# Optimization experiments

Measured on AMD Instinct MI355X. Metric: run time of the kernel, lower is better.

## Reference

```python
import jax, jax.numpy as jnp
import numpy as np

STRIDES = (8, 16, 32)
BINS = 16
NC = 80
ALPHA, GAMMA = 0.25, 2.0
W_CLS, W_IOU, W_DFL = 1.0, 7.5, 1.5
B, MAX_GT = 32, 32
EPS = 1e-7


def setup_inputs() -> dict:
    key = jax.random.key(0)
    k0, k1, k2, k3, k4, k5, k6 = jax.random.split(key, 7)
    p0 = jax.random.normal(k0, (B, 4 * BINS + NC, 80, 80), dtype=jnp.float32)
    p1 = jax.random.normal(k1, (B, 4 * BINS + NC, 40, 40), dtype=jnp.float32)
    p2 = jax.random.normal(k2, (B, 4 * BINS + NC, 20, 20), dtype=jnp.float32)
    # realistic xyxy boxes inside a 640x640 image
    c = jax.random.uniform(k3, (B, MAX_GT, 2), minval=60.0, maxval=580.0)
    wh = jax.random.uniform(k4, (B, MAX_GT, 2), minval=16.0, maxval=120.0)
    gt_bboxes = jnp.concatenate([c - wh / 2, c + wh / 2], axis=-1).astype(jnp.float32)
    gt_labels = jax.random.randint(k5, (B, MAX_GT), 0, NC, dtype=jnp.int32)
    raw = jax.random.randint(k6, (B, 8400), 0, 20 * MAX_GT, dtype=jnp.int32)
    matched_gt_inds = jnp.where(raw < MAX_GT, raw, -1)
    return {"p0": p0, "p1": p1, "p2": p2, "gt_bboxes": gt_bboxes,
            "gt_labels": gt_labels, "matched_gt_inds": matched_gt_inds}


def _decode_scale(p, stride):
    # p: [B, 4*BINS + NC, H, W]
    Bp, C, H, W = p.shape
    dfl = p[:, :4 * BINS].reshape(Bp, 4, BINS, H, W)
    cls = p[:, 4 * BINS:]
    # DFL decode: expectation of softmax over bins, scaled by stride
    prob = jax.nn.softmax(dfl, axis=2)
    proj = jnp.arange(BINS, dtype=p.dtype)
    dist = jnp.einsum('bkchw,c->bkhw', prob, proj) * stride  # [B,4,H,W] in pixels
    ys, xs = jnp.meshgrid(jnp.arange(H), jnp.arange(W), indexing='ij')
    cx = ((xs.astype(p.dtype)) + 0.5) * stride
    cy = ((ys.astype(p.dtype)) + 0.5) * stride
    boxes = jnp.stack([cx - dist[:, 0], cy - dist[:, 1],
                       cx + dist[:, 2], cy + dist[:, 3]], axis=-1).reshape(Bp, H * W, 4)
    cls_logits = cls.transpose(0, 2, 3, 1).reshape(Bp, H * W, NC)
    dfl_flat = dfl.transpose(0, 3, 4, 1, 2).reshape(Bp, H * W, 4, BINS)
    grid = jnp.stack([cx, cy], axis=-1).reshape(H * W, 2)
    smap = jnp.full((H * W,), stride, dtype=p.dtype)
    return cls_logits, dfl_flat, boxes, grid, smap


def reference(p0, p1, p2, gt_bboxes, gt_labels, matched_gt_inds):
    outs = [_decode_scale(p, s) for p, s in zip((p0, p1, p2), STRIDES)]
    scores = jnp.concatenate([o[0] for o in outs], axis=1)   # [B,N,NC]
    dfl = jnp.concatenate([o[1] for o in outs], axis=1)      # [B,N,4,BINS]
    pboxes = jnp.concatenate([o[2] for o in outs], axis=1)   # [B,N,4]
    grid = jnp.concatenate([o[3] for o in outs], axis=0)     # [N,2]
    smap = jnp.concatenate([o[4] for o in outs], axis=0)     # [N]

    pos = matched_gt_inds >= 0                               # [B,N]
    idx = jnp.where(pos, matched_gt_inds, 0)
    lbl = jnp.take_along_axis(gt_labels, idx, axis=1)        # [B,N]
    posf = pos.astype(scores.dtype)
    tgt_scores = jax.nn.one_hot(lbl, NC, dtype=scores.dtype) * posf[..., None]

    # sigmoid focal loss (stable BCE-with-logits)
    prob = jax.nn.sigmoid(scores)
    ce = jnp.maximum(scores, 0) - scores * tgt_scores + jnp.log1p(jnp.exp(-jnp.abs(scores)))
    p_t = prob * tgt_scores + (1 - prob) * (1 - tgt_scores)
    alpha_t = tgt_scores * ALPHA + (1 - tgt_scores) * (1 - ALPHA)
    cls_elem = alpha_t * (1.0 - p_t) ** GAMMA * ce
    num_pos = jnp.maximum(posf.sum(), 1.0)
    loss_cls = cls_elem.sum() / num_pos

    # gather matched GT boxes per anchor
    tboxes = jnp.take_along_axis(gt_bboxes, idx[..., None], axis=1)  # [B,N,4]
    gx, gy = grid[None, :, 0], grid[None, :, 1]
    l = jnp.clip(gx - tboxes[..., 0], 0.0)
    t = jnp.clip(gy - tboxes[..., 1], 0.0)
    r = jnp.clip(tboxes[..., 2] - gx, 0.0)
    b_ = jnp.clip(tboxes[..., 3] - gy, 0.0)
    dists = jnp.stack([l, t, r, b_], axis=-1) / smap[None, :, None]   # [B,N,4]
    tb = jnp.clip(dists, 0.0, BINS - 1 - 1e-6)
    lo = jnp.floor(tb).astype(jnp.int32)
    hi = jnp.minimum(lo + 1, BINS - 1)
    a = tb - lo.astype(tb.dtype)
    # soft two-bin DFL target (vectorized form of the scatter_add loop)
    tdist = (jax.nn.one_hot(lo, BINS, dtype=dfl.dtype) * (1.0 - a)[..., None]
             + jax.nn.one_hot(hi, BINS, dtype=dfl.dtype) * a[..., None])   # [B,N,4,BINS]
    logp = jax.nn.log_softmax(dfl, axis=-1)
    dfl_elem = -(tdist * logp).sum(-1)                                # [B,N,4]
    loss_dfl = (dfl_elem * posf[..., None]).sum() / (num_pos * 4.0)

    # IoU loss on positives
    ix1 = jnp.maximum(pboxes[..., 0], tboxes[..., 0])
    iy1 = jnp.maximum(pboxes[..., 1], tboxes[..., 1])
    ix2 = jnp.minimum(pboxes[..., 2], tboxes[..., 2])
    iy2 = jnp.minimum(pboxes[..., 3], tboxes[..., 3])
    inter = jnp.clip(ix2 - ix1, 0.0) * jnp.clip(iy2 - iy1, 0.0)
    area_p = jnp.clip(pboxes[..., 2] - pboxes[..., 0], 0.0) * jnp.clip(pboxes[..., 3] - pboxes[..., 1], 0.0)
    area_t = jnp.clip(tboxes[..., 2] - tboxes[..., 0], 0.0) * jnp.clip(tboxes[..., 3] - tboxes[..., 1], 0.0)
    iou = inter / (area_p + area_t - inter + EPS)
    loss_iou = ((1.0 - iou) * posf).sum() / num_pos

    total = W_CLS * loss_cls + W_IOU * loss_iou + W_DFL * loss_dfl
    return total
```

## Files before the change

kernel.cpp:

```cpp
#include <hip/hip_runtime.h>
#include <math.h>

#define NCLS 80
#define BINS 16
#define BATCH 32
#define MAX_GT 32
#define NA 8400
#define AN (BATCH * NA)
#define NT 2100
#define NB_CLS 5120
#define NB_DFL 525
#define DFL_THREADS (NB_DFL * 256)
#define NSLOT 64
#define ALPHA_C 0.25f
#define W_CLS 1.0
#define W_IOU 7.5
#define W_DFL 1.5
#define EPS_F 1e-7f


__device__ __forceinline__ void block_reduce_atomic(float val, double* __restrict__ target)
{
    __shared__ float s[4];
    __syncthreads();
    #pragma unroll
    for (int o = 32; o > 0; o >>= 1) val += __shfl_down(val, o);
    const int wave = threadIdx.x >> 6, lane = threadIdx.x & 63;
    if (lane == 0) s[wave] = val;
    __syncthreads();
    if (threadIdx.x == 0) atomicAdd(target, (double)(s[0] + s[1] + s[2] + s[3]));
}

__global__ __launch_bounds__(256) void yolo_prep(
    const int* __restrict__ matched, const int* __restrict__ gt_labels,
    signed char* __restrict__ lblmap)
{
    const int qid = blockIdx.x * 256 + threadIdx.x;
    if (qid >= AN / 4) return;
    const int a0 = qid * 4;
    const int b  = a0 / NA;
    const int4 m4 = *(const int4*)(matched + a0);
    const int mm[4] = {m4.x, m4.y, m4.z, m4.w};
    char4 o;
    o.x = (mm[0] >= 0) ? (signed char)gt_labels[b * MAX_GT + mm[0]] : (signed char)-1;
    o.y = (mm[1] >= 0) ? (signed char)gt_labels[b * MAX_GT + mm[1]] : (signed char)-1;
    o.z = (mm[2] >= 0) ? (signed char)gt_labels[b * MAX_GT + mm[2]] : (signed char)-1;
    o.w = (mm[3] >= 0) ? (signed char)gt_labels[b * MAX_GT + mm[3]] : (signed char)-1;
    *(char4*)(lblmap + a0) = o;
}

__global__ __launch_bounds__(256) void yolo_mega(
    const float* __restrict__ p0, const float* __restrict__ p1, const float* __restrict__ p2,
    const float* __restrict__ gt_bboxes, const int* __restrict__ matched,
    const signed char* __restrict__ lblmap,
    float* __restrict__ pdist, double* __restrict__ acc)
{
    const int bid  = blockIdx.x;
    const int slot = bid & (NSLOT - 1);
    float part = 0.f;

    if (bid < NB_CLS) {
        const int plane = bid >> 1;
        const int b = plane / NCLS;
        const int c = plane - b * NCLS;

        for (int t = (bid & 1) * 256 + (int)threadIdx.x; t < NT; t += 512) {
            const float* p; int HW, off, gbase;
            if (t < 1600)      { p = p0; HW = 6400; off = t * 4;          gbase = 0;    }
            else if (t < 2000) { p = p1; HW = 1600; off = (t - 1600) * 4; gbase = 6400; }
            else               { p = p2; HW = 400;  off = (t - 2000) * 4; gbase = 8000; }

            float4 q = *(const float4*)(p + (size_t)(b * 144 + 4 * BINS + c) * HW + off);
            char4 l4 = *(const char4*)(lblmap + b * NA + gbase + off);
            const int   lbl[4] = {l4.x, l4.y, l4.z, l4.w};
            const float s4[4]  = {q.x, q.y, q.z, q.w};
            #pragma unroll
            for (int j = 0; j < 4; ++j) {
                float s  = s4[j];
                float tt = (c == lbl[j]) ? 1.f : 0.f;
                float e   = __expf(-fabsf(s));
                float inv = 1.f / (1.f + e);
                float prob = (s >= 0.f) ? inv : e * inv;
                float ce  = fmaxf(s, 0.f) - s * tt + __logf(1.f + e);
                float p_t = prob * tt + (1.f - prob) * (1.f - tt);
                float alpha_t = tt * ALPHA_C + (1.f - tt) * (1.f - ALPHA_C);
                float om = 1.f - p_t;
                part += alpha_t * om * om * ce;
            }
        }
        block_reduce_atomic(part, &acc[0 * NSLOT + slot]);
    } else {
        const int dt0 = (bid - NB_CLS) * 256 + (int)threadIdx.x;
        #pragma unroll
        for (int rep = 0; rep < 2; ++rep) {
            const int it = dt0 + rep * DFL_THREADS;
            const int t  = it % NT;
            const int r  = it / NT;
            const int b  = r & 31;
            const int k  = r >> 5;

            const float* p; int HW, off, gbase, h, w0; float stride;
            if (t < 1600)      { p = p0; HW = 6400; off = t * 4;          gbase = 0;    stride = 8.f;
                                 h = t / 20;  w0 = (t - h * 20) * 4; }
            else if (t < 2000) { p = p1; HW = 1600; off = (t - 1600) * 4; gbase = 6400; stride = 16.f;
                                 int u = t - 1600; h = u / 10; w0 = (u - h * 10) * 4; }
            else               { p = p2; HW = 400;  off = (t - 2000) * 4; gbase = 8000; stride = 32.f;
                                 int u = t - 2000; h = u / 5;  w0 = (u - h * 5) * 4; }
            const float inv_s = 1.f / stride;
            const float cy = ((float)h + 0.5f) * stride;

            const int4 m4 = *(const int4*)(matched + (size_t)b * NA + gbase + off);
            const int mm[4] = {m4.x, m4.y, m4.z, m4.w};

            float tdv[4]; bool pos[4];
            #pragma unroll
            for (int j = 0; j < 4; ++j) {
                pos[j] = (mm[j] >= 0);
                int idx = pos[j] ? mm[j] : 0;
                float4 tb = *(const float4*)(gt_bboxes + ((size_t)b * MAX_GT + idx) * 4);
                float cx = ((float)(w0 + j) + 0.5f) * stride;
                float d = (k == 0) ? (cx - tb.x) : (k == 1) ? (cy - tb.y)
                        : (k == 2) ? (tb.z - cx) : (tb.w - cy);
                tdv[j] = fmaxf(d, 0.f) * inv_s;
            }

            const float* pc = p + (size_t)(b * 144 + k * BINS) * HW + off;
            float v[BINS][4];
            #pragma unroll
            for (int i = 0; i < BINS; ++i) {
                float4 q = *(const float4*)(pc + (size_t)i * HW);
                v[i][0] = q.x; v[i][1] = q.y; v[i][2] = q.z; v[i][3] = q.w;
            }

            float pd[4];
            #pragma unroll
            for (int j = 0; j < 4; ++j) {
                float tval = fminf(tdv[j], (float)(BINS - 1) - 1e-6f);
                int   lo = (int)floorf(tval);
                float fr = tval - (float)lo;

                float mx = v[0][j];
                #pragma unroll
                for (int i = 1; i < BINS; ++i) mx = fmaxf(mx, v[i][j]);

                float se = 0.f, we = 0.f, vlo = 0.f, vhi = 0.f;
                #pragma unroll
                for (int i = 0; i < BINS; ++i) {
                    float e = __expf(v[i][j] - mx);
                    se += e;
                    we += (float)i * e;
                    vlo = (i == lo)     ? v[i][j] : vlo;
                    vhi = (i == lo + 1) ? v[i][j] : vhi;
                }
                pd[j] = (we / se) * stride;
                if (pos[j]) {
                    float lse = mx + __logf(se);
                    part += -((1.f - fr) * (vlo - lse) + fr * (vhi - lse));
                }
            }
            float4 st = {pd[0], pd[1], pd[2], pd[3]};
            *(float4*)(pdist + (size_t)k * AN + (size_t)b * NA + gbase + off) = st;
        }
        block_reduce_atomic(part, &acc[2 * NSLOT + slot]);
    }
}

__global__ __launch_bounds__(256) void yolo_iou(
    const float* __restrict__ gt_bboxes, const int* __restrict__ matched,
    const float* __restrict__ pdist, double* __restrict__ acc)
{
    const int t = blockIdx.x * 256 + threadIdx.x;
    const int b = blockIdx.y;
    const int slot = (blockIdx.x + blockIdx.y * 9) & (NSLOT - 1);

    float iou_acc = 0.f, cnt = 0.f;

    if (t < NT) {
        int HW, W, off, gbase; float stride;
        if (t < 1600)      { HW = 6400; W = 80; stride = 8.f;  off = t * 4;          gbase = 0;    }
        else if (t < 2000) { HW = 1600; W = 40; stride = 16.f; off = (t - 1600) * 4; gbase = 6400; }
        else               { HW = 400;  W = 20; stride = 32.f; off = (t - 2000) * 4; gbase = 8000; }

        const int h  = off / W;
        const int w0 = off - h * W;
        const float cy = ((float)h + 0.5f) * stride;

        const int4 m4 = *(const int4*)(matched + (size_t)b * NA + gbase + off);
        const int mm[4] = {m4.x, m4.y, m4.z, m4.w};

        float pdj[4][4];
        #pragma unroll
        for (int k = 0; k < 4; ++k) {
            float4 q = *(const float4*)(pdist + (size_t)k * AN + (size_t)b * NA + gbase + off);
            pdj[k][0] = q.x; pdj[k][1] = q.y; pdj[k][2] = q.z; pdj[k][3] = q.w;
        }

        #pragma unroll
        for (int j = 0; j < 4; ++j) {
            if (mm[j] >= 0) {
                float4 tb = *(const float4*)(gt_bboxes + ((size_t)b * MAX_GT + mm[j]) * 4);
                float cx = ((float)(w0 + j) + 0.5f) * stride;
                float px1 = cx - pdj[0][j], py1 = cy - pdj[1][j];
                float px2 = cx + pdj[2][j], py2 = cy + pdj[3][j];
                float ix1 = fmaxf(px1, tb.x), iy1 = fmaxf(py1, tb.y);
                float ix2 = fminf(px2, tb.z), iy2 = fminf(py2, tb.w);
                float inter  = fmaxf(ix2 - ix1, 0.f) * fmaxf(iy2 - iy1, 0.f);
                float area_p = fmaxf(px2 - px1, 0.f) * fmaxf(py2 - py1, 0.f);
                float area_t = fmaxf(tb.z - tb.x, 0.f) * fmaxf(tb.w - tb.y, 0.f);
                float iou = inter / (area_p + area_t - inter + EPS_F);
                iou_acc += 1.f - iou;
                cnt += 1.f;
            }
        }
    }
    block_reduce_atomic(iou_acc, &acc[1 * NSLOT + slot]);
    block_reduce_atomic(cnt,     &acc[3 * NSLOT + slot]);
}

__global__ __launch_bounds__(256) void yolo_loss_fused(
    const float* __restrict__ p0, const float* __restrict__ p1, const float* __restrict__ p2,
    const float* __restrict__ gt_bboxes, const int* __restrict__ gt_labels,
    const int* __restrict__ matched, double* __restrict__ acc)
{
    const int a = blockIdx.x * blockDim.x + threadIdx.x;
    const int b = blockIdx.y;
    const int slot = blockIdx.x & (NSLOT - 1);
    float cls_acc = 0.f, iou_acc = 0.f, dfl_acc = 0.f, pos_cnt = 0.f;
    if (a < NA) {
        const float* p; int HW, W; float stride; int off;
        if (a < 6400)      { p = p0; HW = 6400; W = 80; stride = 8.f;  off = a; }
        else if (a < 8000) { p = p1; HW = 1600; W = 40; stride = 16.f; off = a - 6400; }
        else               { p = p2; HW = 400;  W = 20; stride = 32.f; off = a - 8000; }
        const int h = off / W, w = off - h * W;
        const float cx = ((float)w + 0.5f) * stride, cy = ((float)h + 0.5f) * stride;
        const float* pb = p + ((size_t)b * 144) * (size_t)HW + (size_t)off;
        const int m = matched[(size_t)b * NA + a];
        const bool pos = (m >= 0);
        const int idx = pos ? m : 0;
        const int lbl = gt_labels[b * MAX_GT + idx];
        const float* tbp = gt_bboxes + ((size_t)b * MAX_GT + idx) * 4;
        const float tx1 = tbp[0], ty1 = tbp[1], tx2 = tbp[2], ty2 = tbp[3];
        float tdist[4] = {fmaxf(cx - tx1, 0.f) / stride, fmaxf(cy - ty1, 0.f) / stride,
                          fmaxf(tx2 - cx, 0.f) / stride, fmaxf(ty2 - cy, 0.f) / stride};
        float pdv[4]; float dfl_sum = 0.f;
        #pragma unroll
        for (int k = 0; k < 4; ++k) {
            float tv = fminf(tdist[k], (float)(BINS - 1) - 1e-6f);
            int lo = (int)floorf(tv);
            float fr = tv - (float)lo;
            const float* pc = pb + (size_t)(k * BINS) * HW;
            float v[BINS];
            #pragma unroll
            for (int i = 0; i < BINS; ++i) v[i] = pc[(size_t)i * HW];
            float mx = v[0];
            #pragma unroll
            for (int i = 1; i < BINS; ++i) mx = fmaxf(mx, v[i]);
            float se = 0.f, we = 0.f, vlo = 0.f, vhi = 0.f;
            #pragma unroll
            for (int i = 0; i < BINS; ++i) {
                float e = __expf(v[i] - mx);
                se += e; we += (float)i * e;
                vlo = (i == lo) ? v[i] : vlo;
                vhi = (i == lo + 1) ? v[i] : vhi;
            }
            pdv[k] = (we / se) * stride;
            if (pos) { float lse = mx + __logf(se); dfl_sum += -((1.f - fr) * (vlo - lse) + fr * (vhi - lse)); }
        }
        const float* pcls = pb + (size_t)(4 * BINS) * HW;
        #pragma unroll 4
        for (int c = 0; c < NCLS; ++c) {
            float s = pcls[(size_t)c * HW];
            float tt = (pos && c == lbl) ? 1.f : 0.f;
            float e = __expf(-fabsf(s));
            float inv = 1.f / (1.f + e);
            float prob = (s >= 0.f) ? inv : e * inv;
            float ce = fmaxf(s, 0.f) - s * tt + __logf(1.f + e);
            float p_t = prob * tt + (1.f - prob) * (1.f - tt);
            float alpha_t = tt * ALPHA_C + (1.f - tt) * (1.f - ALPHA_C);
            float om = 1.f - p_t;
            cls_acc += alpha_t * om * om * ce;
        }
        if (pos) {
            float px1 = cx - pdv[0], py1 = cy - pdv[1], px2 = cx + pdv[2], py2 = cy + pdv[3];
            float ix1 = fmaxf(px1, tx1), iy1 = fmaxf(py1, ty1);
            float ix2 = fminf(px2, tx2), iy2 = fminf(py2, ty2);
            float inter  = fmaxf(ix2 - ix1, 0.f) * fmaxf(iy2 - iy1, 0.f);
            float area_p = fmaxf(px2 - px1, 0.f) * fmaxf(py2 - py1, 0.f);
            float area_t = fmaxf(tx2 - tx1, 0.f) * fmaxf(ty2 - ty1, 0.f);
            float iou = inter / (area_p + area_t - inter + EPS_F);
            iou_acc = 1.f - iou; dfl_acc = dfl_sum; pos_cnt = 1.f;
        }
    }
    block_reduce_atomic(cls_acc, &acc[0 * NSLOT + slot]);
    block_reduce_atomic(iou_acc, &acc[1 * NSLOT + slot]);
    block_reduce_atomic(dfl_acc, &acc[2 * NSLOT + slot]);
    block_reduce_atomic(pos_cnt, &acc[3 * NSLOT + slot]);
}

__global__ void yolo_loss_finalize(const double* __restrict__ acc, float* __restrict__ out)
{
    double s[4] = {0.0, 0.0, 0.0, 0.0};
    for (int q = 0; q < 4; ++q)
        for (int i = 0; i < NSLOT; ++i) s[q] += acc[q * NSLOT + i];
    double np = s[3] < 1.0 ? 1.0 : s[3];
    double total = W_CLS * s[0] / np + W_IOU * s[1] / np + W_DFL * s[2] / (np * 4.0);
    out[0] = (float)total;
}

extern "C" void kernel_launch(void* const* d_in, const int* in_sizes, int n_in,
                              void* d_out, int out_size, void* d_ws, size_t ws_size,
                              hipStream_t stream)
{
    const float* p0        = (const float*)d_in[0];
    const float* p1        = (const float*)d_in[1];
    const float* p2        = (const float*)d_in[2];
    const float* gt_bboxes = (const float*)d_in[3];
    const int*   gt_labels = (const int*)d_in[4];
    const int*   matched   = (const int*)d_in[5];
    float*  out = (float*)d_out;

    const size_t accBytes   = 4 * NSLOT * sizeof(double);
    const size_t pdistBytes = (size_t)4 * AN * sizeof(float);
    double*      acc    = (double*)d_ws;
    float*       pdist  = (float*)((char*)d_ws + accBytes);
    signed char* lblmap = (signed char*)((char*)d_ws + accBytes + pdistBytes);
    const size_t need = accBytes + pdistBytes + (size_t)AN;

    (void)hipMemsetAsync(acc, 0, accBytes, stream);

    if (ws_size >= need) {
        yolo_prep<<<(AN / 4 + 255) / 256, 256, 0, stream>>>(matched, gt_labels, lblmap);
        yolo_mega<<<NB_CLS + NB_DFL, 256, 0, stream>>>(p0, p1, p2, gt_bboxes, matched,
                                                       lblmap, pdist, acc);
        dim3 g2((NT + 255) / 256, BATCH);
        yolo_iou<<<g2, 256, 0, stream>>>(gt_bboxes, matched, pdist, acc);
    } else {
        dim3 g((NA + 255) / 256, BATCH);
        yolo_loss_fused<<<g, 256, 0, stream>>>(p0, p1, p2, gt_bboxes, gt_labels, matched, acc);
    }
    yolo_loss_finalize<<<1, 1, 0, stream>>>(acc, out);
}
```

Before: 229.4 us.

## Fuse IoU into DFL blocks via shared memory, drop pdist buffer and memset

```diff
diff --git a/kernel.cpp b/kernel.cpp
--- a/kernel.cpp
+++ b/kernel.cpp
@@ -8,9 +8,8 @@
 #define NA 8400
 #define AN (BATCH * NA)
 #define NT 2100
-#define NB_CLS 5120
-#define NB_DFL 525
-#define DFL_THREADS (NB_DFL * 256)
+#define NB_DFL 1050
+#define NB_CLS 2560
 #define NSLOT 64
 #define ALPHA_C 0.25f
 #define W_CLS 1.0
@@ -31,10 +30,23 @@
     if (threadIdx.x == 0) atomicAdd(target, (double)(s[0] + s[1] + s[2] + s[3]));
 }
 
+__device__ __forceinline__ float focal_elem(float s, float tt)
+{
+    float e   = __expf(-fabsf(s));
+    float inv = 1.f / (1.f + e);
+    float prob = (s >= 0.f) ? inv : e * inv;
+    float ce  = fmaxf(s, 0.f) - s * tt + __logf(1.f + e);
+    float p_t = prob * tt + (1.f - prob) * (1.f - tt);
+    float alpha_t = tt * ALPHA_C + (1.f - tt) * (1.f - ALPHA_C);
+    float om = 1.f - p_t;
+    return alpha_t * om * om * ce;
+}
+
 __global__ __launch_bounds__(256) void yolo_prep(
     const int* __restrict__ matched, const int* __restrict__ gt_labels,
-    signed char* __restrict__ lblmap)
-{
+    signed char* __restrict__ lblmap, double* __restrict__ acc)
+{
+    if (blockIdx.x == 0) acc[threadIdx.x] = 0.0;
     const int qid = blockIdx.x * 256 + threadIdx.x;
     if (qid >= AN / 4) return;
     const int a0 = qid * 4;
@@ -52,169 +64,144 @@
 __global__ __launch_bounds__(256) void yolo_mega(
     const float* __restrict__ p0, const float* __restrict__ p1, const float* __restrict__ p2,
     const float* __restrict__ gt_bboxes, const int* __restrict__ matched,
-    const signed char* __restrict__ lblmap,
-    float* __restrict__ pdist, double* __restrict__ acc)
+    const signed char* __restrict__ lblmap, double* __restrict__ acc)
 {
     const int bid  = blockIdx.x;
     const int slot = bid & (NSLOT - 1);
-    float part = 0.f;
-
-    if (bid < NB_CLS) {
-        const int plane = bid >> 1;
-        const int b = plane / NCLS;
-        const int c = plane - b * NCLS;
-
-        for (int t = (bid & 1) * 256 + (int)threadIdx.x; t < NT; t += 512) {
-            const float* p; int HW, off, gbase;
-            if (t < 1600)      { p = p0; HW = 6400; off = t * 4;          gbase = 0;    }
-            else if (t < 2000) { p = p1; HW = 1600; off = (t - 1600) * 4; gbase = 6400; }
-            else               { p = p2; HW = 400;  off = (t - 2000) * 4; gbase = 8000; }
-
-            float4 q = *(const float4*)(p + (size_t)(b * 144 + 4 * BINS + c) * HW + off);
-            char4 l4 = *(const char4*)(lblmap + b * NA + gbase + off);
-            const int   lbl[4] = {l4.x, l4.y, l4.z, l4.w};
-            const float s4[4]  = {q.x, q.y, q.z, q.w};
+
+    if (bid < NB_DFL) {
+        __shared__ float spd[64][4][4];
+        const int gdt = bid * 256 + (int)threadIdx.x;
+        const int k   = gdt & 3;
+        const int qg  = gdt >> 2;
+        const int b   = qg / NT;
+        const int t   = qg - b * NT;
+
+        const float* p; int HW, off, gbase, h, w0; float stride;
+        if (t < 1600)      { p = p0; HW = 6400; off = t * 4;          gbase = 0;    stride = 8.f;
+                             h = t / 20;  w0 = (t - h * 20) * 4; }
+        else if (t < 2000) { p = p1; HW = 1600; off = (t - 1600) * 4; gbase = 6400; stride = 16.f;
+                             int u = t - 1600; h = u / 10; w0 = (u - h * 10) * 4; }
+        else               { p = p2; HW = 400;  off = (t - 2000) * 4; gbase = 8000; stride = 32.f;
+                             int u = t - 2000; h = u / 5;  w0 = (u - h * 5) * 4; }
+        const float inv_s = 1.f / stride;
+        const float cy = ((float)h + 0.5f) * stride;
+
+        const float* pc = p + (size_t)(b * 144 + k * BINS) * HW + off;
+        float v[BINS][4];
+        #pragma unroll
+        for (int i = 0; i < BINS; ++i) {
+            float4 q = *(const float4*)(pc + (size_t)i * HW);
+            v[i][0] = q.x; v[i][1] = q.y; v[i][2] = q.z; v[i][3] = q.w;
+        }
+        const int4 m4 = *(const int4*)(matched + (size_t)b * NA + gbase + off);
+        const int mm[4] = {m4.x, m4.y, m4.z, m4.w};
+        bool pos[4]; float4 tbv[4]; float tdv[4];
+        #pragma unroll
+        for (int j = 0; j < 4; ++j) {
+            pos[j] = (mm[j] >= 0);
+            int idx = pos[j] ? mm[j] : 0;
+            tbv[j] = *(const float4*)(gt_bboxes + ((size_t)b * MAX_GT + idx) * 4);
+            float cx = ((float)(w0 + j) + 0.5f) * stride;
+            float d = (k == 0) ? (cx - tbv[j].x) : (k == 1) ? (cy - tbv[j].y)
+                    : (k == 2) ? (tbv[j].z - cx) : (tbv[j].w - cy);
+            tdv[j] = fmaxf(d, 0.f) * inv_s;
+        }
+
+        float part = 0.f;
+        float pd[4];
+        #pragma unroll
+        for (int j = 0; j < 4; ++j) {
+            float tval = fminf(tdv[j], (float)(BINS - 1) - 1e-6f);
+            int   lo = (int)floorf(tval);
+            float fr = tval - (float)lo;
+            float mx = v[0][j];
+            #pragma unroll
+            for (int i = 1; i < BINS; ++i) mx = fmaxf(mx, v[i][j]);
+            float se = 0.f, we = 0.f, vlo = 0.f, vhi = 0.f;
+            #pragma unroll
+            for (int i = 0; i < BINS; ++i) {
+                float e = __expf(v[i][j] - mx);
+                se += e;
+                we += (float)i * e;
+                vlo = (i == lo)     ? v[i][j] : vlo;
+                vhi = (i == lo + 1) ? v[i][j] : vhi;
+            }
+            pd[j] = (we / se) * stride;
+            if (pos[j]) {
+                float lse = mx + __logf(se);
+                part += -((1.f - fr) * (vlo - lse) + fr * (vhi - lse));
+            }
+        }
+        *(float4*)&spd[threadIdx.x >> 2][k][0] = make_float4(pd[0], pd[1], pd[2], pd[3]);
+        __syncthreads();
+
+        float iou_part = 0.f, cnt = 0.f;
+        if (k == 0) {
+            const int g = threadIdx.x >> 2;
             #pragma unroll
             for (int j = 0; j < 4; ++j) {
-                float s  = s4[j];
-                float tt = (c == lbl[j]) ? 1.f : 0.f;
-                float e   = __expf(-fabsf(s));
-                float inv = 1.f / (1.f + e);
-                float prob = (s >= 0.f) ? inv : e * inv;
-                float ce  = fmaxf(s, 0.f) - s * tt + __logf(1.f + e);
-                float p_t = prob * tt + (1.f - prob) * (1.f - tt);
-                float alpha_t = tt * ALPHA_C + (1.f - tt) * (1.f - ALPHA_C);
-                float om = 1.f - p_t;
-                part += alpha_t * om * om * ce;
-            }
-        }
-        block_reduce_atomic(part, &acc[0 * NSLOT + slot]);
-    } else {
-        const int dt0 = (bid - NB_CLS) * 256 + (int)threadIdx.x;
-        #pragma unroll
-        for (int rep = 0; rep < 2; ++rep) {
-            const int it = dt0 + rep * DFL_THREADS;
-            const int t  = it % NT;
-            const int r  = it / NT;
-            const int b  = r & 31;
-            const int k  = r >> 5;
-
-            const float* p; int HW, off, gbase, h, w0; float stride;
-            if (t < 1600)      { p = p0; HW = 6400; off = t * 4;          gbase = 0;    stride = 8.f;
-                                 h = t / 20;  w0 = (t - h * 20) * 4; }
-            else if (t < 2000) { p = p1; HW = 1600; off = (t - 1600) * 4; gbase = 6400; stride = 16.f;
-                                 int u = t - 1600; h = u / 10; w0 = (u - h * 10) * 4; }
-            else               { p = p2; HW = 400;  off = (t - 2000) * 4; gbase = 8000; stride = 32.f;
-                                 int u = t - 2000; h = u / 5;  w0 = (u - h * 5) * 4; }
-            const float inv_s = 1.f / stride;
-            const float cy = ((float)h + 0.5f) * stride;
-
-            const int4 m4 = *(const int4*)(matched + (size_t)b * NA + gbase + off);
-            const int mm[4] = {m4.x, m4.y, m4.z, m4.w};
-
-            float tdv[4]; bool pos[4];
-            #pragma unroll
-            for (int j = 0; j < 4; ++j) {
-                pos[j] = (mm[j] >= 0);
-                int idx = pos[j] ? mm[j] : 0;
-                float4 tb = *(const float4*)(gt_bboxes + ((size_t)b * MAX_GT + idx) * 4);
-                float cx = ((float)(w0 + j) + 0.5f) * stride;
-                float d = (k == 0) ? (cx - tb.x) : (k == 1) ? (cy - tb.y)
-                        : (k == 2) ? (tb.z - cx) : (tb.w - cy);
-                tdv[j] = fmaxf(d, 0.f) * inv_s;
-            }
-
-            const float* pc = p + (size_t)(b * 144 + k * BINS) * HW + off;
-            float v[BINS][4];
-            #pragma unroll
-            for (int i = 0; i < BINS; ++i) {
-                float4 q = *(const float4*)(pc + (size_t)i * HW);
-                v[i][0] = q.x; v[i][1] = q.y; v[i][2] = q.z; v[i][3] = q.w;
-            }
-
-            float pd[4];
-            #pragma unroll
-            for (int j = 0; j < 4; ++j) {
-                float tval = fminf(tdv[j], (float)(BINS - 1) - 1e-6f);
-                int   lo = (int)floorf(tval);
-                float fr = tval - (float)lo;
-
-                float mx = v[0][j];
-                #pragma unroll
-                for (int i = 1; i < BINS; ++i) mx = fmaxf(mx, v[i][j]);
-
-                float se = 0.f, we = 0.f, vlo = 0.f, vhi = 0.f;
-                #pragma unroll
-                for (int i = 0; i < BINS; ++i) {
-                    float e = __expf(v[i][j] - mx);
-                    se += e;
-                    we += (float)i * e;
-                    vlo = (i == lo)     ? v[i][j] : vlo;
-                    vhi = (i == lo + 1) ? v[i][j] : vhi;
-                }
-                pd[j] = (we / se) * stride;
                 if (pos[j]) {
-                    float lse = mx + __logf(se);
-                    part += -((1.f - fr) * (vlo - lse) + fr * (vhi - lse));
+                    float cx = ((float)(w0 + j) + 0.5f) * stride;
+                    float px1 = cx - spd[g][0][j], py1 = cy - spd[g][1][j];
+                    float px2 = cx + spd[g][2][j], py2 = cy + spd[g][3][j];
+                    float4 tb = tbv[j];
+                    float ix1 = fmaxf(px1, tb.x), iy1 = fmaxf(py1, tb.y);
+                    float ix2 = fminf(px2, tb.z), iy2 = fminf(py2, tb.w);
+                    float inter  = fmaxf(ix2 - ix1, 0.f) * fmaxf(iy2 - iy1, 0.f);
+                    float area_p = fmaxf(px2 - px1, 0.f) * fmaxf(py2 - py1, 0.f);
+                    float area_t = fmaxf(tb.z - tb.x, 0.f) * fmaxf(tb.w - tb.y, 0.f);
+                    float iou = inter / (area_p + area_t - inter + EPS_F);
+                    iou_part += 1.f - iou;
+                    cnt += 1.f;
                 }
             }
-            float4 st = {pd[0], pd[1], pd[2], pd[3]};
-            *(float4*)(pdist + (size_t)k * AN + (size_t)b * NA + gbase + off) = st;
-        }
-        block_reduce_atomic(part, &acc[2 * NSLOT + slot]);
+        }
+        block_reduce_atomic(part,     &acc[2 * NSLOT + slot]);
+        block_reduce_atomic(iou_part, &acc[1 * NSLOT + slot]);
+        block_reduce_atomic(cnt,      &acc[3 * NSLOT + slot]);
+    } else {
+        const int cbid = bid - NB_DFL;
+        const int b = cbid / NCLS;
+        const int c = cbid - b * NCLS;
+        const size_t cls_ch = (size_t)(b * 144 + 4 * BINS + c);
+        const signed char* lb0 = lblmap + b * NA;
+
+        float4 q[9];
+        char4  l4[9];
+        const float* pl0 = p0 + cls_ch * 6400;
+        #pragma unroll
+        for (int i = 0; i < 6; ++i) {
+            int off = (i * 256 + (int)threadIdx.x) * 4;
+            q[i]  = *(const float4*)(pl0 + off);
+            l4[i] = *(const char4*)(lb0 + off);
+        }
+        #pragma unroll
+        for (int i = 6; i < 9; ++i) {
+            int t  = i * 256 + (int)threadIdx.x;
+            int tc = (t < NT) ? t : 0;
+            const float* p; int HW, off, gbase;
+            if (tc < 1600)      { p = p0; HW = 6400; off = tc * 4;          gbase = 0;    }
+            else if (tc < 2000) { p = p1; HW = 1600; off = (tc - 1600) * 4; gbase = 6400; }
+            else                { p = p2; HW = 400;  off = (tc - 2000) * 4; gbase = 8000; }
+            q[i]  = *(const float4*)(p + cls_ch * HW + off);
+            l4[i] = *(const char4*)(lb0 + gbase + off);
+        }
+
+        float part = 0.f;
+        #pragma unroll
+        for (int i = 0; i < 9; ++i) {
+            const bool valid = (i < 8) || (i * 256 + (int)threadIdx.x < NT);
+            const float s4[4]  = {q[i].x, q[i].y, q[i].z, q[i].w};
+            const int   lbl[4] = {l4[i].x, l4[i].y, l4[i].z, l4[i].w};
+            float sum = 0.f;
+            #pragma unroll
+            for (int j = 0; j < 4; ++j)
+                sum += focal_elem(s4[j], (c == lbl[j]) ? 1.f : 0.f);
+            part += valid ? sum : 0.f;
+        }
+        block_reduce_atomic(part, &acc[0 * NSLOT + slot]);
     }
-}
-
-__global__ __launch_bounds__(256) void yolo_iou(
-    const float* __restrict__ gt_bboxes, const int* __restrict__ matched,
-    const float* __restrict__ pdist, double* __restrict__ acc)
-{
-    const int t = blockIdx.x * 256 + threadIdx.x;
-    const int b = blockIdx.y;
-    const int slot = (blockIdx.x + blockIdx.y * 9) & (NSLOT - 1);
-
-    float iou_acc = 0.f, cnt = 0.f;
-
-    if (t < NT) {
-        int HW, W, off, gbase; float stride;
-        if (t < 1600)      { HW = 6400; W = 80; stride = 8.f;  off = t * 4;          gbase = 0;    }
-        else if (t < 2000) { HW = 1600; W = 40; stride = 16.f; off = (t - 1600) * 4; gbase = 6400; }
-        else               { HW = 400;  W = 20; stride = 32.f; off = (t - 2000) * 4; gbase = 8000; }
-
-        const int h  = off / W;
-        const int w0 = off - h * W;
-        const float cy = ((float)h + 0.5f) * stride;
-
-        const int4 m4 = *(const int4*)(matched + (size_t)b * NA + gbase + off);
-        const int mm[4] = {m4.x, m4.y, m4.z, m4.w};
-
-        float pdj[4][4];
-        #pragma unroll
-        for (int k = 0; k < 4; ++k) {
-            float4 q = *(const float4*)(pdist + (size_t)k * AN + (size_t)b * NA + gbase + off);
-            pdj[k][0] = q.x; pdj[k][1] = q.y; pdj[k][2] = q.z; pdj[k][3] = q.w;
-        }
-
-        #pragma unroll
-        for (int j = 0; j < 4; ++j) {
-            if (mm[j] >= 0) {
-                float4 tb = *(const float4*)(gt_bboxes + ((size_t)b * MAX_GT + mm[j]) * 4);
-                float cx = ((float)(w0 + j) + 0.5f) * stride;
-                float px1 = cx - pdj[0][j], py1 = cy - pdj[1][j];
-                float px2 = cx + pdj[2][j], py2 = cy + pdj[3][j];
-                float ix1 = fmaxf(px1, tb.x), iy1 = fmaxf(py1, tb.y);
-                float ix2 = fminf(px2, tb.z), iy2 = fminf(py2, tb.w);
-                float inter  = fmaxf(ix2 - ix1, 0.f) * fmaxf(iy2 - iy1, 0.f);
-                float area_p = fmaxf(px2 - px1, 0.f) * fmaxf(py2 - py1, 0.f);
-                float area_t = fmaxf(tb.z - tb.x, 0.f) * fmaxf(tb.w - tb.y, 0.f);
-                float iou = inter / (area_p + area_t - inter + EPS_F);
-                iou_acc += 1.f - iou;
-                cnt += 1.f;
-            }
-        }
-    }
-    block_reduce_atomic(iou_acc, &acc[1 * NSLOT + slot]);
-    block_reduce_atomic(cnt,     &acc[3 * NSLOT + slot]);
 }
 
 __global__ __launch_bounds__(256) void yolo_loss_fused(
@@ -268,18 +255,8 @@
         }
         const float* pcls = pb + (size_t)(4 * BINS) * HW;
         #pragma unroll 4
-        for (int c = 0; c < NCLS; ++c) {
-            float s = pcls[(size_t)c * HW];
-            float tt = (pos && c == lbl) ? 1.f : 0.f;
-            float e = __expf(-fabsf(s));
-            float inv = 1.f / (1.f + e);
-            float prob = (s >= 0.f) ? inv : e * inv;
-            float ce = fmaxf(s, 0.f) - s * tt + __logf(1.f + e);
-            float p_t = prob * tt + (1.f - prob) * (1.f - tt);
-            float alpha_t = tt * ALPHA_C + (1.f - tt) * (1.f - ALPHA_C);
-            float om = 1.f - p_t;
-            cls_acc += alpha_t * om * om * ce;
-        }
+        for (int c = 0; c < NCLS; ++c)
+            cls_acc += focal_elem(pcls[(size_t)c * HW], (pos && c == lbl) ? 1.f : 0.f);
         if (pos) {
             float px1 = cx - pdv[0], py1 = cy - pdv[1], px2 = cx + pdv[2], py2 = cy + pdv[3];
             float ix1 = fmaxf(px1, tx1), iy1 = fmaxf(py1, ty1);
@@ -319,22 +296,17 @@
     const int*   matched   = (const int*)d_in[5];
     float*  out = (float*)d_out;
 
-    const size_t accBytes   = 4 * NSLOT * sizeof(double);
-    const size_t pdistBytes = (size_t)4 * AN * sizeof(float);
+    const size_t accBytes = 4 * NSLOT * sizeof(double);
     double*      acc    = (double*)d_ws;
-    float*       pdist  = (float*)((char*)d_ws + accBytes);
-    signed char* lblmap = (signed char*)((char*)d_ws + accBytes + pdistBytes);
-    const size_t need = accBytes + pdistBytes + (size_t)AN;
-
-    (void)hipMemsetAsync(acc, 0, accBytes, stream);
+    signed char* lblmap = (signed char*)((char*)d_ws + accBytes);
+    const size_t need = accBytes + (size_t)AN;
 
     if (ws_size >= need) {
-        yolo_prep<<<(AN / 4 + 255) / 256, 256, 0, stream>>>(matched, gt_labels, lblmap);
-        yolo_mega<<<NB_CLS + NB_DFL, 256, 0, stream>>>(p0, p1, p2, gt_bboxes, matched,
-                                                       lblmap, pdist, acc);
-        dim3 g2((NT + 255) / 256, BATCH);
-        yolo_iou<<<g2, 256, 0, stream>>>(gt_bboxes, matched, pdist, acc);
+        yolo_prep<<<(AN / 4 + 255) / 256, 256, 0, stream>>>(matched, gt_labels, lblmap, acc);
+        yolo_mega<<<NB_DFL + NB_CLS, 256, 0, stream>>>(p0, p1, p2, gt_bboxes, matched,
+                                                       lblmap, acc);
     } else {
+        (void)hipMemsetAsync(acc, 0, accBytes, stream);
         dim3 g((NA + 255) / 256, BATCH);
         yolo_loss_fused<<<g, 256, 0, stream>>>(p0, p1, p2, gt_bboxes, gt_labels, matched, acc);
     }
```

New measurement: 213.5 us. 1.07x faster.
